# Kernel optimization log

Hardware: AMD Instinct MI355X
Metric: run time of the kernel (lower is better)

Reference implementation:

```python
import jax, jax.numpy as jnp
import numpy as np

D_MODEL = 1024
NUM_HEADS = 16
HEAD_DIM = D_MODEL // NUM_HEADS
R = 1.0
LAM = 0.1
CLIP_MIN = -15.0
CLIP_MAX = 15.0
EPS = 1e-9


def setup_inputs() -> dict:
    key = jax.random.key(0)
    k1, k2 = jax.random.split(key, 2)
    B, S = 2, 2048
    x = jax.random.normal(k1, (B, S, D_MODEL), dtype=jnp.float32)
    # NonNeg-constrained dense kernel -> nonnegative uniform init (small scale)
    W = jax.random.uniform(k2, (D_MODEL, D_MODEL), dtype=jnp.float32) * 0.02
    b = jnp.zeros((D_MODEL,), dtype=jnp.float32)
    d_q = jnp.ones((D_MODEL,), dtype=jnp.float32)
    d_k = jnp.ones((D_MODEL,), dtype=jnp.float32)
    d_v = jnp.ones((D_MODEL,), dtype=jnp.float32)
    return {"x": x, "W": W, "b": b, "d_q": d_q, "d_k": d_k, "d_v": d_v}


def _convex_r_softmax(z):
    z = jnp.clip(z, CLIP_MIN, CLIP_MAX)
    numerator = jax.nn.relu(jnp.exp(z - R) + LAM * z)
    denominator = jnp.sum(numerator, axis=-1, keepdims=True) + EPS
    return numerator / denominator


def reference(x, W, b, d_q, d_k, d_v):
    B, S, _ = x.shape
    x_proj = x @ W + b                      # [B, S, D]
    # diagonal scaling then split heads: [B, H, S, Dh]
    def heads(t):
        return t.reshape(B, S, NUM_HEADS, HEAD_DIM).transpose(0, 2, 1, 3)
    Q = heads(x_proj * d_q)
    K = heads(x_proj * d_k)
    V = heads(x_proj * d_v)
    scores = jnp.einsum('bhqd,bhkd->bhqk', Q, K)   # [B, H, S, S]
    attn = _convex_r_softmax(scores)
    out = jnp.einsum('bhqk,bhkd->bhqd', attn, V)   # [B, H, S, Dh]
    return out.transpose(0, 2, 1, 3).reshape(B, S, D_MODEL)
```

## Files before the change

### kernel.cpp

```cpp
#include <hip/hip_runtime.h>
#include <math.h>

#define D_MODEL   1024
#define NUM_HEADS 16
#define HEAD_DIM  64
#define S_LEN     2048
#define BATCH     2
#define M_TOT     (BATCH * S_LEN)

typedef __attribute__((ext_vector_type(8))) short short8;
typedef __attribute__((ext_vector_type(4))) short short4v;
typedef __attribute__((ext_vector_type(4))) float f32x4;

static __device__ __forceinline__ short f2bf(float f) {
    unsigned u = __builtin_bit_cast(unsigned, f);
    unsigned r = (u + 0x7FFFu + ((u >> 16) & 1u)) >> 16;
    return (short)r;
}

typedef __attribute__((address_space(3))) void lds_v;
typedef const __attribute__((address_space(1))) void glb_v;
static __device__ __forceinline__ void gll16(const void* g, void* l) {
    __builtin_amdgcn_global_load_lds((glb_v*)g, (lds_v*)l, 16, 0, 0);
}


__global__ __launch_bounds__(256) void cvt_xw_kernel(
    const float* __restrict__ x, short* __restrict__ xb,
    const float* __restrict__ W, short* __restrict__ wt)
{
    __shared__ short T[64][72];
    const int bx = blockIdx.x;
    if (bx < 2048) {
        int i = (bx * 256 + threadIdx.x) * 8;
        float4 a = *(const float4*)(x + i);
        float4 b = *(const float4*)(x + i + 4);
        short8 o;
        o[0] = f2bf(a.x); o[1] = f2bf(a.y); o[2] = f2bf(a.z); o[3] = f2bf(a.w);
        o[4] = f2bf(b.x); o[5] = f2bf(b.y); o[6] = f2bf(b.z); o[7] = f2bf(b.w);
        *(short8*)(xb + i) = o;
    } else {
        const int t = bx - 2048;
        const int tid = threadIdx.x;
        const int k0 = (t >> 4) * 64, n0 = (t & 15) * 64;
        const int r = tid >> 4, c4 = (tid & 15) * 4;
        #pragma unroll
        for (int i = 0; i < 4; i++) {
            int kr = r + 16 * i;
            float4 v = *(const float4*)(W + (size_t)(k0 + kr) * D_MODEL + n0 + c4);
            short4v s;
            s[0] = f2bf(v.x); s[1] = f2bf(v.y); s[2] = f2bf(v.z); s[3] = f2bf(v.w);
            *(short4v*)&T[kr][c4] = s;
        }
        __syncthreads();
        const int n = tid >> 2, kb = (tid & 3) * 16;
        short tmp[16];
        #pragma unroll
        for (int j = 0; j < 16; j++) tmp[j] = T[kb + j][n];
        *(short8*)(wt + (size_t)(n0 + n) * D_MODEL + k0 + kb)     = *(short8*)&tmp[0];
        *(short8*)(wt + (size_t)(n0 + n) * D_MODEL + k0 + kb + 8) = *(short8*)&tmp[8];
    }
}

__global__ __launch_bounds__(256) void gemm_qkv_kernel(
    const short* __restrict__ xb, const short* __restrict__ wt,
    const float* __restrict__ bias, const float* __restrict__ dq,
    const float* __restrict__ dk, const float* __restrict__ dv,
    short* __restrict__ Q, short* __restrict__ K, short* __restrict__ Vt)
{
    __shared__ __attribute__((aligned(16))) short lds[12288];

    const int tid  = threadIdx.x;
    const int w    = tid >> 6, l = tid & 63;
    const int quad = l >> 4,  c = l & 15;
    const int cx   = c & 7;
    const int n0 = blockIdx.x * 128, m0 = blockIdx.y * 64;
    const int wm = (w & 1) * 32, wn = (w >> 1) * 64;
    short* As = lds;
    short* Bs = lds + 4096;

    const int srow  = l >> 3;
    const int sslot = (l & 7) ^ srow;

    f32x4 acc[2][4];
    #pragma unroll
    for (int mi = 0; mi < 2; mi++)
        #pragma unroll
        for (int ni = 0; ni < 4; ni++) acc[mi][ni] = (f32x4){0.f, 0.f, 0.f, 0.f};

    for (int k0 = 0; k0 < D_MODEL; k0 += 64) {
        __syncthreads();
        #pragma unroll
        for (int i = 0; i < 2; i++) {
            int rbase = 16 * w + 8 * i;
            gll16(xb + (size_t)(m0 + rbase + srow) * D_MODEL + k0 + sslot * 8,
                  As + rbase * 64);
        }
        #pragma unroll
        for (int i = 0; i < 4; i++) {
            int rbase = 32 * w + 8 * i;
            gll16(wt + (size_t)(n0 + rbase + srow) * D_MODEL + k0 + sslot * 8,
                  Bs + rbase * 64);
        }
        __syncthreads();
        #pragma unroll
        for (int kh = 0; kh < 2; kh++) {
            const int sx = (kh * 4 + quad) ^ cx;
            short8 af[2], bf[4];
            #pragma unroll
            for (int mi = 0; mi < 2; mi++)
                af[mi] = *(const short8*)&As[(wm + 16 * mi + c) * 64 + sx * 8];
            #pragma unroll
            for (int ni = 0; ni < 4; ni++)
                bf[ni] = *(const short8*)&Bs[(wn + 16 * ni + c) * 64 + sx * 8];
            #pragma unroll
            for (int mi = 0; mi < 2; mi++)
                #pragma unroll
                for (int ni = 0; ni < 4; ni++)
                    acc[mi][ni] = __builtin_amdgcn_mfma_f32_16x16x32_bf16(
                        af[mi], bf[ni], acc[mi][ni], 0, 0, 0);
        }
    }

    __syncthreads();
    const int b      = m0 >> 11;
    const int s_base = m0 & 2047;
    const int h      = (n0 + wn) >> 6;

    float biasv[4], dqv[4], dkv[4], dvv[4];
    #pragma unroll
    for (int ni = 0; ni < 4; ni++) {
        int n_g = n0 + wn + 16 * ni + c;
        biasv[ni] = bias[n_g]; dqv[ni] = dq[n_g];
        dkv[ni] = dk[n_g];     dvv[ni] = dv[n_g];
    }

    short* E = lds;
    #pragma unroll
    for (int mi = 0; mi < 2; mi++) {
        #pragma unroll
        for (int ni = 0; ni < 4; ni++) {
            short4v vv;
            #pragma unroll
            for (int r = 0; r < 4; r++) {
                float xv = acc[mi][ni][r] + biasv[ni];
                int s = s_base + wm + 16 * mi + 4 * quad + r;
                size_t off = (((size_t)(b * NUM_HEADS + h) * S_LEN + s) << 6) + (16 * ni + c);
                Q[off] = f2bf(xv * dqv[ni]);
                K[off] = f2bf(xv * dkv[ni]);
                vv[r]  = f2bf(xv * dvv[ni]);
            }
            int n_l = wn + 16 * ni + c;
            int m_l = wm + 16 * mi + 4 * quad;
            *(short4v*)&E[n_l * 72 + m_l] = vv;
        }
    }
    __syncthreads();
    {
        const int n_l = tid >> 1, mh = (tid & 1) * 32;
        const int h2 = (n0 + n_l) >> 6;
        const int dh = n_l & 63;
        short* dst = Vt + ((size_t)(b * NUM_HEADS + h2) * HEAD_DIM + dh) * S_LEN + s_base;
        #pragma unroll
        for (int ch = 0; ch < 4; ch++) {
            short8 v = *(const short8*)&E[n_l * 72 + mh + ch * 8];
            *(short8*)(dst + mh + ch * 8) = v;
        }
    }
}

__global__ __launch_bounds__(256) void attn_split_kernel(
    const short* __restrict__ Q, const short* __restrict__ K,
    const short* __restrict__ Vt, float* __restrict__ Opart,
    float* __restrict__ dpart)
{
    __shared__ __attribute__((aligned(16))) short lds[8192 + 4 * 32 * 88];

    const int tid  = threadIdx.x;
    const int w    = tid >> 6, l = tid & 63;
    const int quad = l >> 4,  c = l & 15;
    const int cx   = c & 7;
    const int qt    = blockIdx.x >> 1;
    const int split = blockIdx.x & 1;
    const int q0 = qt * 128;
    const int h  = blockIdx.y, b = blockIdx.z;
    const size_t bh = (size_t)(b * NUM_HEADS + h);
    const short* Qh  = Q  + bh * S_LEN * HEAD_DIM;
    const short* Kh  = K  + bh * S_LEN * HEAD_DIM;
    const short* Vth = Vt + bh * HEAD_DIM * S_LEN;

    short* Ks = lds;
    short* Vs = lds + 4096;
    short* Ps = lds + 8192 + w * (32 * 88);

    const int srow  = l >> 3;
    const int sslot = (l & 7) ^ srow;

    short8 qf0[2], qf1[2];
    {
        const short* qp0 = Qh + (size_t)(q0 + 32 * w + c) * 64 + quad * 8;
        const short* qp1 = qp0 + 16 * 64;
        qf0[0] = *(const short8*)(qp0);
        qf0[1] = *(const short8*)(qp0 + 32);
        qf1[0] = *(const short8*)(qp1);
        qf1[1] = *(const short8*)(qp1 + 32);
    }

    short8 ones;
    #pragma unroll
    for (int j = 0; j < 8; j++) ones[j] = (short)0x3F80;

    f32x4 o0[4], o1[4], d0a, d1a;
    #pragma unroll
    for (int i = 0; i < 4; i++) {
        o0[i] = (f32x4){0.f, 0.f, 0.f, 0.f};
        o1[i] = (f32x4){0.f, 0.f, 0.f, 0.f};
    }
    d0a = (f32x4){0.f, 0.f, 0.f, 0.f};
    d1a = (f32x4){0.f, 0.f, 0.f, 0.f};

    const int kt_beg = split * (S_LEN / 128);
    for (int kt = kt_beg; kt < kt_beg + S_LEN / 128; kt++) {
        const int k0 = kt * 64;
        __syncthreads();
        #pragma unroll
        for (int i = 0; i < 2; i++) {
            int rbase = 16 * w + 8 * i;
            int row = rbase + srow;
            gll16(Kh + (size_t)(k0 + row) * 64 + sslot * 8, Ks + rbase * 64);
            gll16(Vth + (size_t)row * S_LEN + k0 + sslot * 8, Vs + rbase * 64);
        }
        __syncthreads();

        f32x4 s0[4], s1[4];
        #pragma unroll
        for (int n = 0; n < 4; n++) {
            s0[n] = (f32x4){0.f, 0.f, 0.f, 0.f};
            s1[n] = (f32x4){0.f, 0.f, 0.f, 0.f};
        }
        #pragma unroll
        for (int hh = 0; hh < 2; hh++) {
            const int sx = (hh * 4 + quad) ^ cx;
            #pragma unroll
            for (int n = 0; n < 4; n++) {
                short8 kf = *(const short8*)&Ks[(16 * n + c) * 64 + sx * 8];
                s0[n] = __builtin_amdgcn_mfma_f32_16x16x32_bf16(kf, qf0[hh], s0[n], 0, 0, 0);
                s1[n] = __builtin_amdgcn_mfma_f32_16x16x32_bf16(kf, qf1[hh], s1[n], 0, 0, 0);
            }
        }

        #pragma unroll
        for (int n = 0; n < 4; n++) {
            float nm[4];
            #pragma unroll
            for (int r = 0; r < 4; r++) {
                float z = __builtin_amdgcn_fmed3f(s0[n][r], -15.0f, 15.0f);
                float e = __builtin_amdgcn_exp2f(
                    __builtin_fmaf(z, 1.4426950408889634f, -1.4426950408889634f));
                nm[r] = fmaxf(__builtin_fmaf(z, 0.1f, e), 0.0f);
            }
            unsigned p0 = __builtin_amdgcn_perm(
                __builtin_bit_cast(unsigned, nm[1]) + 0x8000u,
                __builtin_bit_cast(unsigned, nm[0]) + 0x8000u, 0x07060302u);
            unsigned p1 = __builtin_amdgcn_perm(
                __builtin_bit_cast(unsigned, nm[3]) + 0x8000u,
                __builtin_bit_cast(unsigned, nm[2]) + 0x8000u, 0x07060302u);
            uint2 pr; pr.x = p0; pr.y = p1;
            *(uint2*)&Ps[c * 88 + 16 * n + 4 * quad] = pr;
        }
        #pragma unroll
        for (int n = 0; n < 4; n++) {
            float nm[4];
            #pragma unroll
            for (int r = 0; r < 4; r++) {
                float z = __builtin_amdgcn_fmed3f(s1[n][r], -15.0f, 15.0f);
                float e = __builtin_amdgcn_exp2f(
                    __builtin_fmaf(z, 1.4426950408889634f, -1.4426950408889634f));
                nm[r] = fmaxf(__builtin_fmaf(z, 0.1f, e), 0.0f);
            }
            unsigned p0 = __builtin_amdgcn_perm(
                __builtin_bit_cast(unsigned, nm[1]) + 0x8000u,
                __builtin_bit_cast(unsigned, nm[0]) + 0x8000u, 0x07060302u);
            unsigned p1 = __builtin_amdgcn_perm(
                __builtin_bit_cast(unsigned, nm[3]) + 0x8000u,
                __builtin_bit_cast(unsigned, nm[2]) + 0x8000u, 0x07060302u);
            uint2 pr; pr.x = p0; pr.y = p1;
            *(uint2*)&Ps[(16 + c) * 88 + 16 * n + 4 * quad] = pr;
        }

        #pragma unroll
        for (int kh = 0; kh < 2; kh++) {
            short8 pf0 = *(const short8*)&Ps[c * 88 + 32 * kh + 8 * quad];
            short8 pf1 = *(const short8*)&Ps[(16 + c) * 88 + 32 * kh + 8 * quad];
            const int sx = (kh * 4 + quad) ^ cx;
            #pragma unroll
            for (int n2 = 0; n2 < 4; n2++) {
                short8 vf = *(const short8*)&Vs[(16 * n2 + c) * 64 + sx * 8];
                o0[n2] = __builtin_amdgcn_mfma_f32_16x16x32_bf16(pf0, vf, o0[n2], 0, 0, 0);
                o1[n2] = __builtin_amdgcn_mfma_f32_16x16x32_bf16(pf1, vf, o1[n2], 0, 0, 0);
            }
            d0a = __builtin_amdgcn_mfma_f32_16x16x32_bf16(pf0, ones, d0a, 0, 0, 0);
            d1a = __builtin_amdgcn_mfma_f32_16x16x32_bf16(pf1, ones, d1a, 0, 0, 0);
        }
    }

    float* Op = Opart + ((((size_t)split * BATCH + b) * NUM_HEADS + h) * 16 + qt) * (128 * 64);
    float* dp = dpart + ((((size_t)split * BATCH + b) * NUM_HEADS + h) * 16 + qt) * 128;

    #pragma unroll
    for (int r = 0; r < 4; r++) {
        int row0 = 32 * w + 4 * quad + r;
        #pragma unroll
        for (int n2 = 0; n2 < 4; n2++) {
            Op[row0 * 64 + 16 * n2 + c]        = o0[n2][r];
            Op[(row0 + 16) * 64 + 16 * n2 + c] = o1[n2][r];
        }
        if (c == 0) {
            dp[row0]      = d0a[r];
            dp[row0 + 16] = d1a[r];
        }
    }
}

__global__ __launch_bounds__(256) void combine_kernel(
    const float* __restrict__ Opart, const float* __restrict__ dpart,
    float* __restrict__ out)
{
    const int gid = blockIdx.x * 256 + threadIdx.x;
    const int row = gid >> 4;
    const int col = (gid & 15) * 4;
    float d = dpart[row] + dpart[65536 + row] + 1e-9f;
    float inv = 1.0f / d;
    float4 a = *(const float4*)(Opart + (size_t)gid * 4);
    float4 bb = *(const float4*)(Opart + 4194304 + (size_t)gid * 4);
    const int b = row >> 15;
    const int h = (row >> 11) & 15;
    const int s = row & 2047;
    float4 r;
    r.x = (a.x + bb.x) * inv; r.y = (a.y + bb.y) * inv;
    r.z = (a.z + bb.z) * inv; r.w = (a.w + bb.w) * inv;
    *(float4*)(out + ((size_t)(b * S_LEN + s) << 10) + (h << 6) + col) = r;
}

__global__ __launch_bounds__(256) void attn2_kernel(
    const short* __restrict__ Q, const short* __restrict__ K,
    const short* __restrict__ Vt, float* __restrict__ out)
{
    __shared__ __attribute__((aligned(16))) short lds[8192 + 4 * 32 * 88];

    const int tid  = threadIdx.x;
    const int w    = tid >> 6, l = tid & 63;
    const int quad = l >> 4,  c = l & 15;
    const int cx   = c & 7;
    const int q0 = blockIdx.x * 128;
    const int h  = blockIdx.y, b = blockIdx.z;
    const size_t bh = (size_t)(b * NUM_HEADS + h);
    const short* Qh  = Q  + bh * S_LEN * HEAD_DIM;
    const short* Kh  = K  + bh * S_LEN * HEAD_DIM;
    const short* Vth = Vt + bh * HEAD_DIM * S_LEN;

    short* Ks = lds;
    short* Vs = lds + 4096;
    short* Ps = lds + 8192 + w * (32 * 88);

    const int srow  = l >> 3;
    const int sslot = (l & 7) ^ srow;

    short8 qf0[2], qf1[2];
    {
        const short* qp0 = Qh + (size_t)(q0 + 32 * w + c) * 64 + quad * 8;
        const short* qp1 = qp0 + 16 * 64;
        qf0[0] = *(const short8*)(qp0);
        qf0[1] = *(const short8*)(qp0 + 32);
        qf1[0] = *(const short8*)(qp1);
        qf1[1] = *(const short8*)(qp1 + 32);
    }

    f32x4 o0[4], o1[4];
    #pragma unroll
    for (int i = 0; i < 4; i++) {
        o0[i] = (f32x4){0.f, 0.f, 0.f, 0.f};
        o1[i] = (f32x4){0.f, 0.f, 0.f, 0.f};
    }
    float dnm0 = 0.0f, dnm1 = 0.0f;

    for (int kt = 0; kt < S_LEN / 64; kt++) {
        const int k0 = kt * 64;
        __syncthreads();
        #pragma unroll
        for (int i = 0; i < 2; i++) {
            int rbase = 16 * w + 8 * i;
            int row = rbase + srow;
            gll16(Kh + (size_t)(k0 + row) * 64 + sslot * 8, Ks + rbase * 64);
            gll16(Vth + (size_t)row * S_LEN + k0 + sslot * 8, Vs + rbase * 64);
        }
        __syncthreads();

        f32x4 s0[4], s1[4];
        #pragma unroll
        for (int n = 0; n < 4; n++) {
            s0[n] = (f32x4){0.f, 0.f, 0.f, 0.f};
            s1[n] = (f32x4){0.f, 0.f, 0.f, 0.f};
        }
        #pragma unroll
        for (int hh = 0; hh < 2; hh++) {
            const int sx = (hh * 4 + quad) ^ cx;
            #pragma unroll
            for (int n = 0; n < 4; n++) {
                short8 kf = *(const short8*)&Ks[(16 * n + c) * 64 + sx * 8];
                s0[n] = __builtin_amdgcn_mfma_f32_16x16x32_bf16(kf, qf0[hh], s0[n], 0, 0, 0);
                s1[n] = __builtin_amdgcn_mfma_f32_16x16x32_bf16(kf, qf1[hh], s1[n], 0, 0, 0);
            }
        }

        #pragma unroll
        for (int n = 0; n < 4; n++) {
            float nm[4];
            #pragma unroll
            for (int r = 0; r < 4; r++) {
                float z = __builtin_amdgcn_fmed3f(s0[n][r], -15.0f, 15.0f);
                float e = __builtin_amdgcn_exp2f(
                    __builtin_fmaf(z, 1.4426950408889634f, -1.4426950408889634f));
                float num = fmaxf(__builtin_fmaf(z, 0.1f, e), 0.0f);
                dnm0 += num;
                nm[r] = num;
            }
            unsigned p0 = __builtin_amdgcn_perm(
                __builtin_bit_cast(unsigned, nm[1]) + 0x8000u,
                __builtin_bit_cast(unsigned, nm[0]) + 0x8000u, 0x07060302u);
            unsigned p1 = __builtin_amdgcn_perm(
                __builtin_bit_cast(unsigned, nm[3]) + 0x8000u,
                __builtin_bit_cast(unsigned, nm[2]) + 0x8000u, 0x07060302u);
            uint2 pr; pr.x = p0; pr.y = p1;
            *(uint2*)&Ps[c * 88 + 16 * n + 4 * quad] = pr;
        }
        #pragma unroll
        for (int n = 0; n < 4; n++) {
            float nm[4];
            #pragma unroll
            for (int r = 0; r < 4; r++) {
                float z = __builtin_amdgcn_fmed3f(s1[n][r], -15.0f, 15.0f);
                float e = __builtin_amdgcn_exp2f(
                    __builtin_fmaf(z, 1.4426950408889634f, -1.4426950408889634f));
                float num = fmaxf(__builtin_fmaf(z, 0.1f, e), 0.0f);
                dnm1 += num;
                nm[r] = num;
            }
            unsigned p0 = __builtin_amdgcn_perm(
                __builtin_bit_cast(unsigned, nm[1]) + 0x8000u,
                __builtin_bit_cast(unsigned, nm[0]) + 0x8000u, 0x07060302u);
            unsigned p1 = __builtin_amdgcn_perm(
                __builtin_bit_cast(unsigned, nm[3]) + 0x8000u,
                __builtin_bit_cast(unsigned, nm[2]) + 0x8000u, 0x07060302u);
            uint2 pr; pr.x = p0; pr.y = p1;
            *(uint2*)&Ps[(16 + c) * 88 + 16 * n + 4 * quad] = pr;
        }

        #pragma unroll
        for (int kh = 0; kh < 2; kh++) {
            short8 pf0 = *(const short8*)&Ps[c * 88 + 32 * kh + 8 * quad];
            short8 pf1 = *(const short8*)&Ps[(16 + c) * 88 + 32 * kh + 8 * quad];
            const int sx = (kh * 4 + quad) ^ cx;
            #pragma unroll
            for (int n2 = 0; n2 < 4; n2++) {
                short8 vf = *(const short8*)&Vs[(16 * n2 + c) * 64 + sx * 8];
                o0[n2] = __builtin_amdgcn_mfma_f32_16x16x32_bf16(pf0, vf, o0[n2], 0, 0, 0);
                o1[n2] = __builtin_amdgcn_mfma_f32_16x16x32_bf16(pf1, vf, o1[n2], 0, 0, 0);
            }
        }
    }

    dnm0 += __shfl_xor(dnm0, 16, 64);
    dnm0 += __shfl_xor(dnm0, 32, 64);
    dnm1 += __shfl_xor(dnm1, 16, 64);
    dnm1 += __shfl_xor(dnm1, 32, 64);

    #pragma unroll
    for (int r = 0; r < 4; r++) {
        float dr0 = __shfl(dnm0, quad * 4 + r, 64);
        float dr1 = __shfl(dnm1, quad * 4 + r, 64);
        float inv0 = 1.0f / (dr0 + 1e-9f);
        float inv1 = 1.0f / (dr1 + 1e-9f);
        int qrow0 = q0 + 32 * w + 4 * quad + r;
        float* op0 = out + ((size_t)(b * S_LEN + qrow0) << 10) + (h << 6) + c;
        float* op1 = op0 + (16 << 10);
        #pragma unroll
        for (int n2 = 0; n2 < 4; n2++) {
            op0[16 * n2] = o0[n2][r] * inv0;
            op1[16 * n2] = o1[n2][r] * inv1;
        }
    }
}

__global__ __launch_bounds__(256, 4) void gemm_xw_kernel(
    const float* __restrict__ x, const float* __restrict__ W,
    const float* __restrict__ bias, float* __restrict__ xp)
{
    __shared__ float Asf[64][36];
    __shared__ float Bsf[32][68];

    const int tid = threadIdx.x;
    const int tx  = tid & 15;
    const int ty  = tid >> 4;
    const int m0  = blockIdx.y * 64;
    const int n0  = blockIdx.x * 64;

    float acc[4][4];
    #pragma unroll
    for (int i = 0; i < 4; i++)
        #pragma unroll
        for (int j = 0; j < 4; j++) acc[i][j] = 0.0f;

    for (int k0 = 0; k0 < D_MODEL; k0 += 32) {
        #pragma unroll
        for (int i = 0; i < 2; i++) {
            int idx = tid + i * 256;
            int r = idx >> 3, c4 = idx & 7;
            *(float4*)(&Asf[r][c4 * 4]) =
                *(const float4*)(x + (size_t)(m0 + r) * D_MODEL + k0 + c4 * 4);
        }
        #pragma unroll
        for (int i = 0; i < 2; i++) {
            int idx = tid + i * 256;
            int r = idx >> 4, c4 = idx & 15;
            *(float4*)(&Bsf[r][c4 * 4]) =
                *(const float4*)(W + (size_t)(k0 + r) * D_MODEL + n0 + c4 * 4);
        }
        __syncthreads();
        #pragma unroll
        for (int k = 0; k < 32; k += 4) {
            float a[4][4];
            #pragma unroll
            for (int i = 0; i < 4; i++) {
                float4 t = *(const float4*)(&Asf[ty + 16 * i][k]);
                a[i][0] = t.x; a[i][1] = t.y; a[i][2] = t.z; a[i][3] = t.w;
            }
            #pragma unroll
            for (int kk = 0; kk < 4; kk++) {
                float4 bv = *(const float4*)(&Bsf[k + kk][tx * 4]);
                #pragma unroll
                for (int i = 0; i < 4; i++) {
                    acc[i][0] += a[i][kk] * bv.x;
                    acc[i][1] += a[i][kk] * bv.y;
                    acc[i][2] += a[i][kk] * bv.z;
                    acc[i][3] += a[i][kk] * bv.w;
                }
            }
        }
        __syncthreads();
    }
    float4 bv = *(const float4*)(bias + n0 + tx * 4);
    #pragma unroll
    for (int i = 0; i < 4; i++) {
        float4 r;
        r.x = acc[i][0] + bv.x; r.y = acc[i][1] + bv.y;
        r.z = acc[i][2] + bv.z; r.w = acc[i][3] + bv.w;
        *(float4*)(xp + (size_t)(m0 + ty + 16 * i) * D_MODEL + n0 + tx * 4) = r;
    }
}

__global__ __launch_bounds__(256, 4) void attn_fb_kernel(
    const float* __restrict__ xp, const float* __restrict__ dq,
    const float* __restrict__ dk, const float* __restrict__ dv,
    float* __restrict__ out)
{
    __shared__ __attribute__((aligned(16))) short lds[13824];

    const int tid  = threadIdx.x;
    const int wave = tid >> 6;
    const int l    = tid & 63;
    const int quad = l >> 4;
    const int c    = l & 15;
    const int q0   = blockIdx.x * 64;
    const int h    = blockIdx.y;
    const int bb   = blockIdx.z;
    const int col0 = h * HEAD_DIM;
    const float* base = xp + (size_t)bb * S_LEN * D_MODEL;

    short* Ks = lds;
    short* Vt = lds + 64 * 72;
    short* Ps = lds + 2 * 64 * 72 + wave * (16 * 72);

    short8 qf[2];
    {
        const int qrow = q0 + wave * 16 + c;
        const float* qp = base + (size_t)qrow * D_MODEL + col0 + quad * 8;
        const float* sp = dq + col0 + quad * 8;
        #pragma unroll
        for (int hh = 0; hh < 2; hh++) {
            float4 v0 = *(const float4*)(qp + 32 * hh);
            float4 v1 = *(const float4*)(qp + 32 * hh + 4);
            float4 s0 = *(const float4*)(sp + 32 * hh);
            float4 s1 = *(const float4*)(sp + 32 * hh + 4);
            qf[hh][0] = f2bf(v0.x * s0.x); qf[hh][1] = f2bf(v0.y * s0.y);
            qf[hh][2] = f2bf(v0.z * s0.z); qf[hh][3] = f2bf(v0.w * s0.w);
            qf[hh][4] = f2bf(v1.x * s1.x); qf[hh][5] = f2bf(v1.y * s1.y);
            qf[hh][6] = f2bf(v1.z * s1.z); qf[hh][7] = f2bf(v1.w * s1.w);
        }
    }

    const int sc4  = 4 * (tid & 15);
    const int srow = tid >> 4;
    const float4 ksc = *(const float4*)(dk + col0 + sc4);
    const int vd = tid & 63;
    const int vg = tid >> 6;
    const float vsc = dv[col0 + vd];

    f32x4 acc_o[4];
    #pragma unroll
    for (int i = 0; i < 4; i++) acc_o[i] = (f32x4){0.f, 0.f, 0.f, 0.f};
    float dnm = 0.0f;

    for (int kt = 0; kt < S_LEN / 64; kt++) {
        const int k0 = kt * 64;
        __syncthreads();

        #pragma unroll
        for (int i = 0; i < 4; i++) {
            int r = srow + 16 * i;
            float4 v = *(const float4*)(base + (size_t)(k0 + r) * D_MODEL + col0 + sc4);
            short4v s;
            s[0] = f2bf(v.x * ksc.x); s[1] = f2bf(v.y * ksc.y);
            s[2] = f2bf(v.z * ksc.z); s[3] = f2bf(v.w * ksc.w);
            *(short4v*)&Ks[r * 72 + sc4] = s;
        }
        #pragma unroll
        for (int p = 0; p < 4; p++) {
            int kb = 16 * p + 4 * vg;
            const float* vp = base + (size_t)(k0 + kb) * D_MODEL + col0 + vd;
            float a0 = vp[0 * D_MODEL], a1 = vp[1 * D_MODEL];
            float a2 = vp[2 * D_MODEL], a3 = vp[3 * D_MODEL];
            short4v s;
            s[0] = f2bf(a0 * vsc); s[1] = f2bf(a1 * vsc);
            s[2] = f2bf(a2 * vsc); s[3] = f2bf(a3 * vsc);
            *(short4v*)&Vt[vd * 72 + kb] = s;
        }
        __syncthreads();

        f32x4 sacc[4];
        #pragma unroll
        for (int n = 0; n < 4; n++) sacc[n] = (f32x4){0.f, 0.f, 0.f, 0.f};
        #pragma unroll
        for (int n = 0; n < 4; n++)
            #pragma unroll
            for (int hh = 0; hh < 2; hh++) {
                short8 kf = *(const short8*)&Ks[(16 * n + c) * 72 + 32 * hh + 8 * quad];
                sacc[n] = __builtin_amdgcn_mfma_f32_16x16x32_bf16(kf, qf[hh], sacc[n], 0, 0, 0);
            }

        #pragma unroll
        for (int n = 0; n < 4; n++) {
            short4v pp;
            #pragma unroll
            for (int r = 0; r < 4; r++) {
                float z = fminf(fmaxf(sacc[n][r], -15.0f), 15.0f);
                float e = __expf(z - 1.0f);
                float num = fmaxf(fmaf(z, 0.1f, e), 0.0f);
                dnm += num;
                pp[r] = f2bf(num);
            }
            *(short4v*)&Ps[c * 72 + 16 * n + 4 * quad] = pp;
        }

        #pragma unroll
        for (int kh = 0; kh < 2; kh++) {
            short8 pf = *(const short8*)&Ps[c * 72 + 32 * kh + 8 * quad];
            #pragma unroll
            for (int n2 = 0; n2 < 4; n2++) {
                short8 vf = *(const short8*)&Vt[(16 * n2 + c) * 72 + 32 * kh + 8 * quad];
                acc_o[n2] = __builtin_amdgcn_mfma_f32_16x16x32_bf16(pf, vf, acc_o[n2], 0, 0, 0);
            }
        }
    }

    dnm += __shfl_xor(dnm, 16, 64);
    dnm += __shfl_xor(dnm, 32, 64);

    #pragma unroll
    for (int r = 0; r < 4; r++) {
        float dr  = __shfl(dnm, quad * 4 + r, 64);
        float inv = 1.0f / (dr + 1e-9f);
        const int qrow = q0 + wave * 16 + quad * 4 + r;
        float* op = out + (size_t)(bb * S_LEN + qrow) * D_MODEL + col0 + c;
        #pragma unroll
        for (int n2 = 0; n2 < 4; n2++)
            op[16 * n2] = acc_o[n2][r] * inv;
    }
}

extern "C" void kernel_launch(void* const* d_in, const int* in_sizes, int n_in,
                              void* d_out, int out_size, void* d_ws, size_t ws_size,
                              hipStream_t stream) {
    const float* x  = (const float*)d_in[0];
    const float* W  = (const float*)d_in[1];
    const float* bias = (const float*)d_in[2];
    const float* dq = (const float*)d_in[3];
    const float* dk = (const float*)d_in[4];
    const float* dv = (const float*)d_in[5];
    float* out = (float*)d_out;

    const size_t XB_B = (size_t)M_TOT * D_MODEL * 2;
    const size_t WT_B = (size_t)D_MODEL * D_MODEL * 2;
    const size_t T_B  = (size_t)BATCH * NUM_HEADS * S_LEN * HEAD_DIM * 2;
    const size_t OP_B = (size_t)2 * 65536 * 64 * 4;
    const size_t DP_B = (size_t)2 * 65536 * 4;
    const size_t NEED1 = XB_B + WT_B + 3 * T_B;
    const size_t NEED2 = NEED1 + OP_B + DP_B;

    if (ws_size >= NEED1) {
        char* p = (char*)d_ws;
        short* xb = (short*)p;             p += XB_B;
        short* wt = (short*)p;             p += WT_B;
        short* Qt = (short*)p;             p += T_B;
        short* Kt = (short*)p;             p += T_B;
        short* Vt = (short*)p;             p += T_B;

        cvt_xw_kernel<<<2048 + 256, 256, 0, stream>>>(x, xb, W, wt);
        dim3 gg(D_MODEL / 128, M_TOT / 64);
        gemm_qkv_kernel<<<gg, 256, 0, stream>>>(xb, wt, bias, dq, dk, dv, Qt, Kt, Vt);

        if (ws_size >= NEED2) {
            float* Opart = (float*)p;      p += OP_B;
            float* dpart = (float*)p;
            dim3 ga(2 * S_LEN / 128, NUM_HEADS, BATCH);
            attn_split_kernel<<<ga, 256, 0, stream>>>(Qt, Kt, Vt, Opart, dpart);
            combine_kernel<<<4096, 256, 0, stream>>>(Opart, dpart, out);
        } else {
            dim3 ga(S_LEN / 128, NUM_HEADS, BATCH);
            attn2_kernel<<<ga, 256, 0, stream>>>(Qt, Kt, Vt, out);
        }
    } else {
        float* xp = (float*)d_ws;
        dim3 g1(D_MODEL / 64, M_TOT / 64);
        gemm_xw_kernel<<<g1, 256, 0, stream>>>(x, W, bias, xp);
        dim3 g2(S_LEN / 64, NUM_HEADS, BATCH);
        attn_fb_kernel<<<g2, 256, 0, stream>>>(xp, dq, dk, dv, out);
    }
}
```

Baseline: 171.5 us.

## Widen QKV GEMM K-tile, store split-attention partials in bf16, add occupancy hint

The QKV GEMM now stages 128-wide K tiles with a 16-slot XOR swizzle, which halves the number of barrier-separated iterations at the cost of doubling LDS use. The split attention kernel writes its partial outputs as bf16 instead of fp32, halving partial-output traffic in it and in the combine kernel. It also computes scores in two halves to lower register pressure and carries a launch_bounds occupancy hint of 4. Storing the partials in bf16 adds rounding error before normalization, and the larger GEMM LDS footprint may reduce occupancy.

```diff
diff --git a/kernel.cpp b/kernel.cpp
--- a/kernel.cpp
+++ b/kernel.cpp
@@ -16,6 +16,9 @@
     unsigned u = __builtin_bit_cast(unsigned, f);
     unsigned r = (u + 0x7FFFu + ((u >> 16) & 1u)) >> 16;
     return (short)r;
+}
+static __device__ __forceinline__ float bf2f(short s) {
+    return __builtin_bit_cast(float, ((unsigned)(unsigned short)s) << 16);
 }
 
 typedef __attribute__((address_space(3))) void lds_v;
@@ -68,19 +71,18 @@
     const float* __restrict__ dk, const float* __restrict__ dv,
     short* __restrict__ Q, short* __restrict__ K, short* __restrict__ Vt)
 {
-    __shared__ __attribute__((aligned(16))) short lds[12288];
+    __shared__ __attribute__((aligned(16))) short lds[24576];
 
     const int tid  = threadIdx.x;
     const int w    = tid >> 6, l = tid & 63;
     const int quad = l >> 4,  c = l & 15;
-    const int cx   = c & 7;
     const int n0 = blockIdx.x * 128, m0 = blockIdx.y * 64;
     const int wm = (w & 1) * 32, wn = (w >> 1) * 64;
     short* As = lds;
-    short* Bs = lds + 4096;
-
-    const int srow  = l >> 3;
-    const int sslot = (l & 7) ^ srow;
+    short* Bs = lds + 8192;
+
+    const int sub  = l >> 4;
+    const int slot = l & 15;
 
     f32x4 acc[2][4];
     #pragma unroll
@@ -88,31 +90,33 @@
         #pragma unroll
         for (int ni = 0; ni < 4; ni++) acc[mi][ni] = (f32x4){0.f, 0.f, 0.f, 0.f};
 
-    for (int k0 = 0; k0 < D_MODEL; k0 += 64) {
-        __syncthreads();
-        #pragma unroll
-        for (int i = 0; i < 2; i++) {
-            int rbase = 16 * w + 8 * i;
-            gll16(xb + (size_t)(m0 + rbase + srow) * D_MODEL + k0 + sslot * 8,
-                  As + rbase * 64);
-        }
+    for (int k0 = 0; k0 < D_MODEL; k0 += 128) {
+        __syncthreads();
         #pragma unroll
         for (int i = 0; i < 4; i++) {
-            int rbase = 32 * w + 8 * i;
-            gll16(wt + (size_t)(n0 + rbase + srow) * D_MODEL + k0 + sslot * 8,
-                  Bs + rbase * 64);
-        }
-        __syncthreads();
-        #pragma unroll
-        for (int kh = 0; kh < 2; kh++) {
-            const int sx = (kh * 4 + quad) ^ cx;
+            int rbase = 16 * w + 4 * i;
+            int row = rbase + sub;
+            int ss = slot ^ (row & 15);
+            gll16(xb + (size_t)(m0 + row) * D_MODEL + k0 + ss * 8, As + rbase * 128);
+        }
+        #pragma unroll
+        for (int i = 0; i < 8; i++) {
+            int rbase = 32 * w + 4 * i;
+            int row = rbase + sub;
+            int ss = slot ^ (row & 15);
+            gll16(wt + (size_t)(n0 + row) * D_MODEL + k0 + ss * 8, Bs + rbase * 128);
+        }
+        __syncthreads();
+        #pragma unroll
+        for (int kh = 0; kh < 4; kh++) {
+            const int sx = (kh * 4 + quad) ^ c;
             short8 af[2], bf[4];
             #pragma unroll
             for (int mi = 0; mi < 2; mi++)
-                af[mi] = *(const short8*)&As[(wm + 16 * mi + c) * 64 + sx * 8];
+                af[mi] = *(const short8*)&As[(wm + 16 * mi + c) * 128 + sx * 8];
             #pragma unroll
             for (int ni = 0; ni < 4; ni++)
-                bf[ni] = *(const short8*)&Bs[(wn + 16 * ni + c) * 64 + sx * 8];
+                bf[ni] = *(const short8*)&Bs[(wn + 16 * ni + c) * 128 + sx * 8];
             #pragma unroll
             for (int mi = 0; mi < 2; mi++)
                 #pragma unroll
@@ -169,9 +173,9 @@
     }
 }
 
-__global__ __launch_bounds__(256) void attn_split_kernel(
+__global__ __launch_bounds__(256, 4) void attn_split_kernel(
     const short* __restrict__ Q, const short* __restrict__ K,
-    const short* __restrict__ Vt, float* __restrict__ Opart,
+    const short* __restrict__ Vt, short* __restrict__ Opart,
     float* __restrict__ dpart)
 {
     __shared__ __attribute__((aligned(16))) short lds[8192 + 4 * 32 * 88];
@@ -232,60 +236,65 @@
         }
         __syncthreads();
 
-        f32x4 s0[4], s1[4];
-        #pragma unroll
-        for (int n = 0; n < 4; n++) {
-            s0[n] = (f32x4){0.f, 0.f, 0.f, 0.f};
-            s1[n] = (f32x4){0.f, 0.f, 0.f, 0.f};
-        }
-        #pragma unroll
-        for (int hh = 0; hh < 2; hh++) {
-            const int sx = (hh * 4 + quad) ^ cx;
-            #pragma unroll
-            for (int n = 0; n < 4; n++) {
-                short8 kf = *(const short8*)&Ks[(16 * n + c) * 64 + sx * 8];
-                s0[n] = __builtin_amdgcn_mfma_f32_16x16x32_bf16(kf, qf0[hh], s0[n], 0, 0, 0);
-                s1[n] = __builtin_amdgcn_mfma_f32_16x16x32_bf16(kf, qf1[hh], s1[n], 0, 0, 0);
-            }
-        }
-
-        #pragma unroll
-        for (int n = 0; n < 4; n++) {
-            float nm[4];
-            #pragma unroll
-            for (int r = 0; r < 4; r++) {
-                float z = __builtin_amdgcn_fmed3f(s0[n][r], -15.0f, 15.0f);
-                float e = __builtin_amdgcn_exp2f(
-                    __builtin_fmaf(z, 1.4426950408889634f, -1.4426950408889634f));
-                nm[r] = fmaxf(__builtin_fmaf(z, 0.1f, e), 0.0f);
-            }
-            unsigned p0 = __builtin_amdgcn_perm(
-                __builtin_bit_cast(unsigned, nm[1]) + 0x8000u,
-                __builtin_bit_cast(unsigned, nm[0]) + 0x8000u, 0x07060302u);
-            unsigned p1 = __builtin_amdgcn_perm(
-                __builtin_bit_cast(unsigned, nm[3]) + 0x8000u,
-                __builtin_bit_cast(unsigned, nm[2]) + 0x8000u, 0x07060302u);
-            uint2 pr; pr.x = p0; pr.y = p1;
-            *(uint2*)&Ps[c * 88 + 16 * n + 4 * quad] = pr;
-        }
-        #pragma unroll
-        for (int n = 0; n < 4; n++) {
-            float nm[4];
-            #pragma unroll
-            for (int r = 0; r < 4; r++) {
-                float z = __builtin_amdgcn_fmed3f(s1[n][r], -15.0f, 15.0f);
-                float e = __builtin_amdgcn_exp2f(
-                    __builtin_fmaf(z, 1.4426950408889634f, -1.4426950408889634f));
-                nm[r] = fmaxf(__builtin_fmaf(z, 0.1f, e), 0.0f);
-            }
-            unsigned p0 = __builtin_amdgcn_perm(
-                __builtin_bit_cast(unsigned, nm[1]) + 0x8000u,
-                __builtin_bit_cast(unsigned, nm[0]) + 0x8000u, 0x07060302u);
-            unsigned p1 = __builtin_amdgcn_perm(
-                __builtin_bit_cast(unsigned, nm[3]) + 0x8000u,
-                __builtin_bit_cast(unsigned, nm[2]) + 0x8000u, 0x07060302u);
-            uint2 pr; pr.x = p0; pr.y = p1;
-            *(uint2*)&Ps[(16 + c) * 88 + 16 * n + 4 * quad] = pr;
+        #pragma unroll
+        for (int nh = 0; nh < 2; nh++) {
+            f32x4 s0[2], s1[2];
+            #pragma unroll
+            for (int nn = 0; nn < 2; nn++) {
+                s0[nn] = (f32x4){0.f, 0.f, 0.f, 0.f};
+                s1[nn] = (f32x4){0.f, 0.f, 0.f, 0.f};
+            }
+            #pragma unroll
+            for (int hh = 0; hh < 2; hh++) {
+                const int sx = (hh * 4 + quad) ^ cx;
+                #pragma unroll
+                for (int nn = 0; nn < 2; nn++) {
+                    const int n = 2 * nh + nn;
+                    short8 kf = *(const short8*)&Ks[(16 * n + c) * 64 + sx * 8];
+                    s0[nn] = __builtin_amdgcn_mfma_f32_16x16x32_bf16(kf, qf0[hh], s0[nn], 0, 0, 0);
+                    s1[nn] = __builtin_amdgcn_mfma_f32_16x16x32_bf16(kf, qf1[hh], s1[nn], 0, 0, 0);
+                }
+            }
+            #pragma unroll
+            for (int nn = 0; nn < 2; nn++) {
+                const int n = 2 * nh + nn;
+                float nm[4];
+                #pragma unroll
+                for (int r = 0; r < 4; r++) {
+                    float z = __builtin_amdgcn_fmed3f(s0[nn][r], -15.0f, 15.0f);
+                    float e = __builtin_amdgcn_exp2f(
+                        __builtin_fmaf(z, 1.4426950408889634f, -1.4426950408889634f));
+                    nm[r] = fmaxf(__builtin_fmaf(z, 0.1f, e), 0.0f);
+                }
+                unsigned p0 = __builtin_amdgcn_perm(
+                    __builtin_bit_cast(unsigned, nm[1]) + 0x8000u,
+                    __builtin_bit_cast(unsigned, nm[0]) + 0x8000u, 0x07060302u);
+                unsigned p1 = __builtin_amdgcn_perm(
+                    __builtin_bit_cast(unsigned, nm[3]) + 0x8000u,
+                    __builtin_bit_cast(unsigned, nm[2]) + 0x8000u, 0x07060302u);
+                uint2 pr; pr.x = p0; pr.y = p1;
+                *(uint2*)&Ps[c * 88 + 16 * n + 4 * quad] = pr;
+            }
+            #pragma unroll
+            for (int nn = 0; nn < 2; nn++) {
+                const int n = 2 * nh + nn;
+                float nm[4];
+                #pragma unroll
+                for (int r = 0; r < 4; r++) {
+                    float z = __builtin_amdgcn_fmed3f(s1[nn][r], -15.0f, 15.0f);
+                    float e = __builtin_amdgcn_exp2f(
+                        __builtin_fmaf(z, 1.4426950408889634f, -1.4426950408889634f));
+                    nm[r] = fmaxf(__builtin_fmaf(z, 0.1f, e), 0.0f);
+                }
+                unsigned p0 = __builtin_amdgcn_perm(
+                    __builtin_bit_cast(unsigned, nm[1]) + 0x8000u,
+                    __builtin_bit_cast(unsigned, nm[0]) + 0x8000u, 0x07060302u);
+                unsigned p1 = __builtin_amdgcn_perm(
+                    __builtin_bit_cast(unsigned, nm[3]) + 0x8000u,
+                    __builtin_bit_cast(unsigned, nm[2]) + 0x8000u, 0x07060302u);
+                uint2 pr; pr.x = p0; pr.y = p1;
+                *(uint2*)&Ps[(16 + c) * 88 + 16 * n + 4 * quad] = pr;
+            }
         }
 
         #pragma unroll
@@ -304,7 +313,7 @@
         }
     }
 
-    float* Op = Opart + ((((size_t)split * BATCH + b) * NUM_HEADS + h) * 16 + qt) * (128 * 64);
+    short* Op = Opart + ((((size_t)split * BATCH + b) * NUM_HEADS + h) * 16 + qt) * (128 * 64);
     float* dp = dpart + ((((size_t)split * BATCH + b) * NUM_HEADS + h) * 16 + qt) * 128;
 
     #pragma unroll
@@ -312,8 +321,8 @@
         int row0 = 32 * w + 4 * quad + r;
         #pragma unroll
         for (int n2 = 0; n2 < 4; n2++) {
-            Op[row0 * 64 + 16 * n2 + c]        = o0[n2][r];
-            Op[(row0 + 16) * 64 + 16 * n2 + c] = o1[n2][r];
+            Op[row0 * 64 + 16 * n2 + c]        = f2bf(o0[n2][r]);
+            Op[(row0 + 16) * 64 + 16 * n2 + c] = f2bf(o1[n2][r]);
         }
         if (c == 0) {
             dp[row0]      = d0a[r];
@@ -323,7 +332,7 @@
 }
 
 __global__ __launch_bounds__(256) void combine_kernel(
-    const float* __restrict__ Opart, const float* __restrict__ dpart,
+    const short* __restrict__ Opart, const float* __restrict__ dpart,
     float* __restrict__ out)
 {
     const int gid = blockIdx.x * 256 + threadIdx.x;
@@ -331,14 +340,16 @@
     const int col = (gid & 15) * 4;
     float d = dpart[row] + dpart[65536 + row] + 1e-9f;
     float inv = 1.0f / d;
-    float4 a = *(const float4*)(Opart + (size_t)gid * 4);
-    float4 bb = *(const float4*)(Opart + 4194304 + (size_t)gid * 4);
+    short4v a  = *(const short4v*)(Opart + (size_t)gid * 4);
+    short4v b2 = *(const short4v*)(Opart + 4194304 + (size_t)gid * 4);
     const int b = row >> 15;
     const int h = (row >> 11) & 15;
     const int s = row & 2047;
     float4 r;
-    r.x = (a.x + bb.x) * inv; r.y = (a.y + bb.y) * inv;
-    r.z = (a.z + bb.z) * inv; r.w = (a.w + bb.w) * inv;
+    r.x = (bf2f(a[0]) + bf2f(b2[0])) * inv;
+    r.y = (bf2f(a[1]) + bf2f(b2[1])) * inv;
+    r.z = (bf2f(a[2]) + bf2f(b2[2])) * inv;
+    r.w = (bf2f(a[3]) + bf2f(b2[3])) * inv;
     *(float4*)(out + ((size_t)(b * S_LEN + s) << 10) + (h << 6) + col) = r;
 }
 
@@ -702,7 +713,7 @@
     const size_t XB_B = (size_t)M_TOT * D_MODEL * 2;
     const size_t WT_B = (size_t)D_MODEL * D_MODEL * 2;
     const size_t T_B  = (size_t)BATCH * NUM_HEADS * S_LEN * HEAD_DIM * 2;
-    const size_t OP_B = (size_t)2 * 65536 * 64 * 4;
+    const size_t OP_B = (size_t)2 * 65536 * 64 * 2;
     const size_t DP_B = (size_t)2 * 65536 * 4;
     const size_t NEED1 = XB_B + WT_B + 3 * T_B;
     const size_t NEED2 = NEED1 + OP_B + DP_B;
@@ -720,7 +731,7 @@
         gemm_qkv_kernel<<<gg, 256, 0, stream>>>(xb, wt, bias, dq, dk, dv, Qt, Kt, Vt);
 
         if (ws_size >= NEED2) {
-            float* Opart = (float*)p;      p += OP_B;
+            short* Opart = (short*)p;      p += OP_B;
             float* dpart = (float*)p;
             dim3 ga(2 * S_LEN / 128, NUM_HEADS, BATCH);
             attn_split_kernel<<<ga, 256, 0, stream>>>(Qt, Kt, Vt, Opart, dpart);
```

Measured after the change: 155.7 us. 1.1x faster.
